# Kernel optimization log

Measured on AMD Instinct MI355X. Metric: run time of the kernel, lower is better.

Reference implementation:

```python
import jax, jax.numpy as jnp
import numpy as np

POOL = (2, 2)
STRIDES = (2, 2)


def _maxpool2d(x):
    # NHWC max pooling, VALID padding (matches K.pool2d(..., pool_mode='max'))
    return jax.lax.reduce_window(
        x, -jnp.inf, jax.lax.max,
        window_dimensions=(1, POOL[0], POOL[1], 1),
        window_strides=(1, STRIDES[0], STRIDES[1], 1),
        padding='VALID')


def setup_inputs() -> dict:
    key = jax.random.key(0)
    ks = jax.random.split(key, 8)
    B, H, W, C = 2, 64, 64, 128
    n_out = 32
    n_pool = (H // POOL[0]) * (W // POOL[1]) * C  # 131072
    y = jax.random.normal(ks[0], (B, H, W, C), jnp.float32)
    x_0 = jax.random.normal(ks[1], (B, 16), jnp.float32)
    mid = jax.random.normal(ks[2], (B, H, W, C), jnp.float32)
    rad = jax.random.uniform(ks[3], (B, H, W, C), jnp.float32)
    u_c = mid + rad  # valid interval bounds: l_c <= u_c
    l_c = mid - rad
    w_out_u = jax.random.normal(ks[4], (B, 1, n_pool, n_out), jnp.float32)
    b_out_u = jax.random.normal(ks[5], (B, 1, n_out), jnp.float32)
    w_out_l = jax.random.normal(ks[6], (B, 1, n_pool, n_out), jnp.float32)
    b_out_l = jax.random.normal(ks[7], (B, 1, n_out), jnp.float32)
    return {"y": y, "x_0": x_0, "u_c": u_c, "l_c": l_c,
            "w_out_u": w_out_u, "b_out_u": b_out_u,
            "w_out_l": w_out_l, "b_out_l": b_out_l}


def reference(y, x_0, u_c, l_c, w_out_u, b_out_u, w_out_l, b_out_l):
    # BackwardMaxPooling2D._pooling_function_fast, mode=F_IBP
    B = y.shape[0]
    # b_u_, b_l_: (B, 1, n_pool, 1) constant post-pool bounds
    b_u = _maxpool2d(u_c).reshape(B, 1, -1, 1)
    b_l = _maxpool2d(l_c).reshape(B, 1, -1, 1)
    n_in = int(np.prod(y.shape[1:]))
    n_out = w_out_u.shape[-1]
    # w_out_u_ = concat([0 * flatten(y)] * n_out) -> identically zero weights
    w_zero = jnp.broadcast_to(0.0 * y.reshape(B, 1, n_in, 1), (B, 1, n_in, n_out))
    # fold backward weights into constant biases using interval bounds
    b_out_u_ = (jnp.sum(jnp.maximum(w_out_u, 0.0) * b_u, axis=2)
                + jnp.sum(jnp.minimum(w_out_u, 0.0) * b_l, axis=2)
                + b_out_u)
    b_out_l_ = (jnp.sum(jnp.maximum(w_out_l, 0.0) * b_l, axis=2)
                + jnp.sum(jnp.minimum(w_out_l, 0.0) * b_u, axis=2)
                + b_out_l)
    return (w_zero, b_out_u_, w_zero, b_out_l_)
```

## Files before the change

### kernel.cpp

```cpp
#include <hip/hip_runtime.h>

#define BATCH 2
#define HH 64
#define WW 64
#define CC 128
#define OHH 32
#define OWW 32
#define NPOOL (OHH * OWW * CC)
#define NOUT 32
#define NIN (HH * WW * CC)
#define WZERO ((size_t)BATCH * NIN * NOUT)

#define OFF_BU (WZERO)
#define OFF_BL (2 * WZERO + (size_t)BATCH * NOUT)

#define CHUNKS 1024
#define PPC (NPOOL / CHUNKS)

typedef float vfloat4 __attribute__((ext_vector_type(4)));

__global__ void zero_kernel(vfloat4* __restrict__ out, size_t n4) {
    size_t tid = (size_t)blockIdx.x * blockDim.x + threadIdx.x;
    size_t stride = (size_t)gridDim.x * blockDim.x;
    const vfloat4 z = {0.f, 0.f, 0.f, 0.f};
    for (size_t i = tid; i < n4; i += stride)
        __builtin_nontemporal_store(z, &out[i]);
}

__global__ void pool_kernel(const float4* __restrict__ u_c,
                            const float4* __restrict__ l_c,
                            float4* __restrict__ bu,
                            float4* __restrict__ bl) {
    int tid = blockIdx.x * blockDim.x + threadIdx.x;
    int c4 = tid & 31;
    int ow = (tid >> 5) & 31;
    int oh = (tid >> 10) & 31;
    int b  = tid >> 15;

    int base = ((b * HH + 2 * oh) * WW + 2 * ow) * (CC / 4) + c4;
    const int colstep = CC / 4;
    const int rowstep = WW * (CC / 4);

    {
        float4 a0 = u_c[base];
        float4 a1 = u_c[base + colstep];
        float4 a2 = u_c[base + rowstep];
        float4 a3 = u_c[base + rowstep + colstep];
        float4 m;
        m.x = fmaxf(fmaxf(a0.x, a1.x), fmaxf(a2.x, a3.x));
        m.y = fmaxf(fmaxf(a0.y, a1.y), fmaxf(a2.y, a3.y));
        m.z = fmaxf(fmaxf(a0.z, a1.z), fmaxf(a2.z, a3.z));
        m.w = fmaxf(fmaxf(a0.w, a1.w), fmaxf(a2.w, a3.w));
        bu[tid] = m;
    }
    {
        float4 a0 = l_c[base];
        float4 a1 = l_c[base + colstep];
        float4 a2 = l_c[base + rowstep];
        float4 a3 = l_c[base + rowstep + colstep];
        float4 m;
        m.x = fmaxf(fmaxf(a0.x, a1.x), fmaxf(a2.x, a3.x));
        m.y = fmaxf(fmaxf(a0.y, a1.y), fmaxf(a2.y, a3.y));
        m.z = fmaxf(fmaxf(a0.z, a1.z), fmaxf(a2.z, a3.z));
        m.w = fmaxf(fmaxf(a0.w, a1.w), fmaxf(a2.w, a3.w));
        bl[tid] = m;
    }
}

__global__ void reduce_kernel(const vfloat4* __restrict__ wu,
                              const vfloat4* __restrict__ wl,
                              const float* __restrict__ bu,
                              const float* __restrict__ bl,
                              float4* __restrict__ part) {
    int b = blockIdx.x / CHUNKS;
    int chunk = blockIdx.x % CHUNKS;
    int t = threadIdx.x;
    int og = t & 7;
    int pl = t >> 3;

    float4 au = make_float4(0.f, 0.f, 0.f, 0.f);
    float4 al = make_float4(0.f, 0.f, 0.f, 0.f);

    const float* bub = bu + b * NPOOL;
    const float* blb = bl + b * NPOOL;
    int p0 = chunk * PPC;

#pragma unroll
    for (int it = 0; it < PPC / 32; ++it) {
        int p = p0 + pl + it * 32;
        float vbu = bub[p];
        float vbl = blb[p];
        size_t widx = ((size_t)b * NPOOL + p) * (NOUT / 4) + og;
        vfloat4 u4 = __builtin_nontemporal_load(&wu[widx]);
        vfloat4 l4 = __builtin_nontemporal_load(&wl[widx]);
        au.x += fmaxf(u4.x, 0.f) * vbu + fminf(u4.x, 0.f) * vbl;
        au.y += fmaxf(u4.y, 0.f) * vbu + fminf(u4.y, 0.f) * vbl;
        au.z += fmaxf(u4.z, 0.f) * vbu + fminf(u4.z, 0.f) * vbl;
        au.w += fmaxf(u4.w, 0.f) * vbu + fminf(u4.w, 0.f) * vbl;
        al.x += fmaxf(l4.x, 0.f) * vbl + fminf(l4.x, 0.f) * vbu;
        al.y += fmaxf(l4.y, 0.f) * vbl + fminf(l4.y, 0.f) * vbu;
        al.z += fmaxf(l4.z, 0.f) * vbl + fminf(l4.z, 0.f) * vbu;
        al.w += fmaxf(l4.w, 0.f) * vbl + fminf(l4.w, 0.f) * vbu;
    }

    __shared__ float4 su[256];
    __shared__ float4 sl[256];
    su[t] = au;
    sl[t] = al;
    __syncthreads();

    for (int s = 128; s >= 8; s >>= 1) {
        if (t < s) {
            float4 xu = su[t + s];
            su[t].x += xu.x; su[t].y += xu.y; su[t].z += xu.z; su[t].w += xu.w;
            float4 xl = sl[t + s];
            sl[t].x += xl.x; sl[t].y += xl.y; sl[t].z += xl.z; sl[t].w += xl.w;
        }
        __syncthreads();
    }

    if (t < 8) {
        size_t row = ((size_t)b * CHUNKS + chunk) * 16;
        part[row + t] = su[t];
        part[row + 8 + t] = sl[t];
    }
}

__global__ void final_kernel(const float* __restrict__ part,
                             const float* __restrict__ b_out_u,
                             const float* __restrict__ b_out_l,
                             float* __restrict__ out) {
    int j = threadIdx.x;
    int b = j >> 6;
    int slot = j & 63;

    float acc = 0.f;
    const float* p = part + (size_t)b * CHUNKS * 64 + slot;
    for (int c = 0; c < CHUNKS; ++c)
        acc += p[(size_t)c * 64];

    if (slot < 32) {
        out[OFF_BU + b * NOUT + slot] = acc + b_out_u[b * NOUT + slot];
    } else {
        int o = slot - 32;
        out[OFF_BL + b * NOUT + o] = acc + b_out_l[b * NOUT + o];
    }
}

extern "C" void kernel_launch(void* const* d_in, const int* in_sizes, int n_in,
                              void* d_out, int out_size, void* d_ws, size_t ws_size,
                              hipStream_t stream) {
    const float* u_c     = (const float*)d_in[2];
    const float* l_c     = (const float*)d_in[3];
    const float* w_out_u = (const float*)d_in[4];
    const float* b_out_u = (const float*)d_in[5];
    const float* w_out_l = (const float*)d_in[6];
    const float* b_out_l = (const float*)d_in[7];
    float* out = (float*)d_out;

    float* ws_bu = (float*)d_ws;
    float* ws_bl = ws_bu + (size_t)BATCH * NPOOL;
    float* ws_part = ws_bl + (size_t)BATCH * NPOOL;

    size_t n4 = (size_t)out_size / 4;
    zero_kernel<<<4096, 256, 0, stream>>>((vfloat4*)out, n4);

    pool_kernel<<<256, 256, 0, stream>>>(
        (const float4*)u_c, (const float4*)l_c,
        (float4*)ws_bu, (float4*)ws_bl);

    reduce_kernel<<<BATCH * CHUNKS, 256, 0, stream>>>(
        (const vfloat4*)w_out_u, (const vfloat4*)w_out_l,
        ws_bu, ws_bl, (float4*)ws_part);

    final_kernel<<<1, 128, 0, stream>>>(ws_part, b_out_u, b_out_l, out);
}
```

Before: 367.5 us.

## Fuse zero-fill, max-pool and weighted reduction into one kernel launch

After: 359.5 us. -2.2%, faster.

```diff
diff --git a/kernel.cpp b/kernel.cpp
--- a/kernel.cpp
+++ b/kernel.cpp
@@ -16,81 +16,73 @@
 
 #define CHUNKS 1024
 #define PPC (NPOOL / CHUNKS)
+#define RBLOCKS (BATCH * CHUNKS)
+#define ZBLOCKS 4096
+#define NTHREADS 256
 
 typedef float vfloat4 __attribute__((ext_vector_type(4)));
 
-__global__ void zero_kernel(vfloat4* __restrict__ out, size_t n4) {
-    size_t tid = (size_t)blockIdx.x * blockDim.x + threadIdx.x;
-    size_t stride = (size_t)gridDim.x * blockDim.x;
-    const vfloat4 z = {0.f, 0.f, 0.f, 0.f};
-    for (size_t i = tid; i < n4; i += stride)
-        __builtin_nontemporal_store(z, &out[i]);
-}
+__global__ void __launch_bounds__(NTHREADS)
+fused_kernel(const float* __restrict__ u_c,
+             const float* __restrict__ l_c,
+             const vfloat4* __restrict__ wu,
+             const vfloat4* __restrict__ wl,
+             vfloat4* __restrict__ outz, size_t n4,
+             float4* __restrict__ part) {
+    int bid = blockIdx.x;
+    int t = threadIdx.x;
 
-__global__ void pool_kernel(const float4* __restrict__ u_c,
-                            const float4* __restrict__ l_c,
-                            float4* __restrict__ bu,
-                            float4* __restrict__ bl) {
-    int tid = blockIdx.x * blockDim.x + threadIdx.x;
-    int c4 = tid & 31;
-    int ow = (tid >> 5) & 31;
-    int oh = (tid >> 10) & 31;
-    int b  = tid >> 15;
+    if (bid >= RBLOCKS) {
+        int zb = bid - RBLOCKS;
+        size_t idx = (size_t)zb * NTHREADS + t;
+        const size_t stride = (size_t)ZBLOCKS * NTHREADS;
+        const vfloat4 z = {0.f, 0.f, 0.f, 0.f};
+        for (size_t i = idx; i < n4; i += stride)
+            __builtin_nontemporal_store(z, &outz[i]);
+        return;
+    }
 
-    int base = ((b * HH + 2 * oh) * WW + 2 * ow) * (CC / 4) + c4;
-    const int colstep = CC / 4;
-    const int rowstep = WW * (CC / 4);
+    int rb = bid;
+    int b = rb >> 10;
+    int chunk = rb & (CHUNKS - 1);
+    int oh = chunk >> 5;
+    int ow = chunk & 31;
 
+    __shared__ float s_bu[CC];
+    __shared__ float s_bl[CC];
     {
-        float4 a0 = u_c[base];
-        float4 a1 = u_c[base + colstep];
-        float4 a2 = u_c[base + rowstep];
-        float4 a3 = u_c[base + rowstep + colstep];
-        float4 m;
-        m.x = fmaxf(fmaxf(a0.x, a1.x), fmaxf(a2.x, a3.x));
-        m.y = fmaxf(fmaxf(a0.y, a1.y), fmaxf(a2.y, a3.y));
-        m.z = fmaxf(fmaxf(a0.z, a1.z), fmaxf(a2.z, a3.z));
-        m.w = fmaxf(fmaxf(a0.w, a1.w), fmaxf(a2.w, a3.w));
-        bu[tid] = m;
+        int base = ((b * HH + 2 * oh) * WW + 2 * ow) * CC;
+        if (t < CC) {
+            int c = t;
+            float a0 = u_c[base + c];
+            float a1 = u_c[base + CC + c];
+            float a2 = u_c[base + WW * CC + c];
+            float a3 = u_c[base + WW * CC + CC + c];
+            s_bu[c] = fmaxf(fmaxf(a0, a1), fmaxf(a2, a3));
+        } else {
+            int c = t - CC;
+            float a0 = l_c[base + c];
+            float a1 = l_c[base + CC + c];
+            float a2 = l_c[base + WW * CC + c];
+            float a3 = l_c[base + WW * CC + CC + c];
+            s_bl[c] = fmaxf(fmaxf(a0, a1), fmaxf(a2, a3));
+        }
     }
-    {
-        float4 a0 = l_c[base];
-        float4 a1 = l_c[base + colstep];
-        float4 a2 = l_c[base + rowstep];
-        float4 a3 = l_c[base + rowstep + colstep];
-        float4 m;
-        m.x = fmaxf(fmaxf(a0.x, a1.x), fmaxf(a2.x, a3.x));
-        m.y = fmaxf(fmaxf(a0.y, a1.y), fmaxf(a2.y, a3.y));
-        m.z = fmaxf(fmaxf(a0.z, a1.z), fmaxf(a2.z, a3.z));
-        m.w = fmaxf(fmaxf(a0.w, a1.w), fmaxf(a2.w, a3.w));
-        bl[tid] = m;
-    }
-}
+    __syncthreads();
 
-__global__ void reduce_kernel(const vfloat4* __restrict__ wu,
-                              const vfloat4* __restrict__ wl,
-                              const float* __restrict__ bu,
-                              const float* __restrict__ bl,
-                              float4* __restrict__ part) {
-    int b = blockIdx.x / CHUNKS;
-    int chunk = blockIdx.x % CHUNKS;
-    int t = threadIdx.x;
     int og = t & 7;
     int pl = t >> 3;
 
     float4 au = make_float4(0.f, 0.f, 0.f, 0.f);
     float4 al = make_float4(0.f, 0.f, 0.f, 0.f);
-
-    const float* bub = bu + b * NPOOL;
-    const float* blb = bl + b * NPOOL;
     int p0 = chunk * PPC;
 
 #pragma unroll
     for (int it = 0; it < PPC / 32; ++it) {
-        int p = p0 + pl + it * 32;
-        float vbu = bub[p];
-        float vbl = blb[p];
-        size_t widx = ((size_t)b * NPOOL + p) * (NOUT / 4) + og;
+        int c = pl + it * 32;
+        float vbu = s_bu[c];
+        float vbl = s_bl[c];
+        size_t widx = ((size_t)b * NPOOL + p0 + c) * (NOUT / 4) + og;
         vfloat4 u4 = __builtin_nontemporal_load(&wu[widx]);
         vfloat4 l4 = __builtin_nontemporal_load(&wl[widx]);
         au.x += fmaxf(u4.x, 0.f) * vbu + fminf(u4.x, 0.f) * vbl;
@@ -103,8 +95,8 @@
         al.w += fmaxf(l4.w, 0.f) * vbl + fminf(l4.w, 0.f) * vbu;
     }
 
-    __shared__ float4 su[256];
-    __shared__ float4 sl[256];
+    __shared__ float4 su[NTHREADS];
+    __shared__ float4 sl[NTHREADS];
     su[t] = au;
     sl[t] = al;
     __syncthreads();
@@ -120,7 +112,7 @@
     }
 
     if (t < 8) {
-        size_t row = ((size_t)b * CHUNKS + chunk) * 16;
+        size_t row = (size_t)rb * 16;
         part[row + t] = su[t];
         part[row + 8 + t] = sl[t];
     }
@@ -158,20 +150,14 @@
     const float* b_out_l = (const float*)d_in[7];
     float* out = (float*)d_out;
 
-    float* ws_bu = (float*)d_ws;
-    float* ws_bl = ws_bu + (size_t)BATCH * NPOOL;
-    float* ws_part = ws_bl + (size_t)BATCH * NPOOL;
+    float* ws_part = (float*)d_ws;
 
     size_t n4 = (size_t)out_size / 4;
-    zero_kernel<<<4096, 256, 0, stream>>>((vfloat4*)out, n4);
 
-    pool_kernel<<<256, 256, 0, stream>>>(
-        (const float4*)u_c, (const float4*)l_c,
-        (float4*)ws_bu, (float4*)ws_bl);
-
-    reduce_kernel<<<BATCH * CHUNKS, 256, 0, stream>>>(
+    fused_kernel<<<RBLOCKS + ZBLOCKS, NTHREADS, 0, stream>>>(
+        u_c, l_c,
         (const vfloat4*)w_out_u, (const vfloat4*)w_out_l,
-        ws_bu, ws_bl, (float4*)ws_part);
+        (vfloat4*)out, n4, (float4*)ws_part);
 
     final_kernel<<<1, 128, 0, stream>>>(ws_part, b_out_u, b_out_l, out);
 }
```
